# Kernel tuning notes

Hardware: AMD Instinct MI355X
Metric: run time of the kernel (lower is better)

The kernel has to match this reference:

```python
import jax, jax.numpy as jnp
import numpy as np

B, T, I, H, O = 64, 2048, 256, 256, 128

def _rnn_scan(xp, W_hh):
    # xp: [T, B, H] = precomputed W_ih @ x + b_ih + b_hh per timestep
    h0 = jnp.zeros((xp.shape[1], W_hh.shape[0]), xp.dtype)
    def step(h, xt):
        h_new = jnp.tanh(xt + h @ W_hh.T)
        return h_new, h_new
    _, hs = jax.lax.scan(step, h0, xp)
    return hs  # [T, B, H]

def setup_inputs() -> dict:
    key = jax.random.key(0)
    ks = jax.random.split(key, 9)
    s1 = 1.0 / np.sqrt(H)
    s2 = 1.0 / np.sqrt(O)
    return {
        "x": jax.random.normal(ks[0], (B, T, I), dtype=jnp.float32),
        "W_ih1": jax.random.normal(ks[1], (H, I), dtype=jnp.float32) * s1,
        "W_hh1": jax.random.normal(ks[2], (H, H), dtype=jnp.float32) * s1,
        "b_ih1": jax.random.normal(ks[3], (H,), dtype=jnp.float32) * s1,
        "b_hh1": jax.random.normal(ks[4], (H,), dtype=jnp.float32) * s1,
        "W_ih2": jax.random.normal(ks[5], (O, H), dtype=jnp.float32) * s2,
        "W_hh2": jax.random.normal(ks[6], (O, O), dtype=jnp.float32) * s2,
        "b_ih2": jax.random.normal(ks[7], (O,), dtype=jnp.float32) * s2,
        "b_hh2": jax.random.normal(ks[8], (O,), dtype=jnp.float32) * s2,
    }

def reference(x, W_ih1, W_hh1, b_ih1, b_hh1, W_ih2, W_hh2, b_ih2, b_hh2):
    # Layer 1: h_t = tanh(W_ih1 x_t + b_ih1 + W_hh1 h_{t-1} + b_hh1)
    xp1 = jnp.einsum('bti,hi->tbh', x, W_ih1) + (b_ih1 + b_hh1)
    h1 = _rnn_scan(xp1, W_hh1)                      # [T, B, H]
    # Layer 2: o_t = tanh(W_ih2 h_t + b_ih2 + W_hh2 o_{t-1} + b_hh2)
    xp2 = jnp.einsum('tbh,oh->tbo', h1, W_ih2) + (b_ih2 + b_hh2)
    h2 = _rnn_scan(xp2, W_hh2)                      # [T, B, O]
    out = jnp.transpose(h2, (1, 0, 2)).reshape(-1, O)  # [B*T, num_classes]
    return out
```

## Files before the change

kernel.cpp:

```cpp
#include <hip/hip_runtime.h>
#include <math.h>

#define BB 64
#define TT 2048
#define II 256
#define HH 256
#define OO 128

template<int N>
__global__ __launch_bounds__(256)
void gemm_bias(const float* __restrict__ A, const float* __restrict__ W,
               const float* __restrict__ b1, const float* __restrict__ b2,
               float* __restrict__ C)
{
    constexpr int K = 256;
    __shared__ float sA[16][132];
    __shared__ float sB[16][132];
    const int tid  = threadIdx.x;
    const long row0 = (long)blockIdx.x * 128;
    const int  col0 = blockIdx.y * 128;

    const int tm = tid & 15;
    const int tn = tid >> 4;

    float acc[8][8];
#pragma unroll
    for (int i = 0; i < 8; ++i)
#pragma unroll
        for (int j = 0; j < 8; ++j) acc[i][j] = 0.f;

    const int f0  = tid;
    const int f1  = tid + 256;
    const int am0 = f0 >> 2, ak0 = (f0 & 3) * 4;
    const int am1 = f1 >> 2, ak1 = (f1 & 3) * 4;

    for (int kt = 0; kt < K; kt += 16) {
        float4 a0 = *(const float4*)&A[(row0 + am0) * K + kt + ak0];
        float4 a1 = *(const float4*)&A[(row0 + am1) * K + kt + ak1];
        float4 w0 = *(const float4*)&W[(long)(col0 + am0) * K + kt + ak0];
        float4 w1 = *(const float4*)&W[(long)(col0 + am1) * K + kt + ak1];
        __syncthreads();
        sA[ak0+0][am0] = a0.x; sA[ak0+1][am0] = a0.y; sA[ak0+2][am0] = a0.z; sA[ak0+3][am0] = a0.w;
        sA[ak1+0][am1] = a1.x; sA[ak1+1][am1] = a1.y; sA[ak1+2][am1] = a1.z; sA[ak1+3][am1] = a1.w;
        sB[ak0+0][am0] = w0.x; sB[ak0+1][am0] = w0.y; sB[ak0+2][am0] = w0.z; sB[ak0+3][am0] = w0.w;
        sB[ak1+0][am1] = w1.x; sB[ak1+1][am1] = w1.y; sB[ak1+2][am1] = w1.z; sB[ak1+3][am1] = w1.w;
        __syncthreads();
#pragma unroll
        for (int k = 0; k < 16; ++k) {
            float4 av0 = *(const float4*)&sA[k][tm * 8];
            float4 av1 = *(const float4*)&sA[k][tm * 8 + 4];
            float4 bv0 = *(const float4*)&sB[k][tn * 8];
            float4 bv1 = *(const float4*)&sB[k][tn * 8 + 4];
            float am[8] = {av0.x, av0.y, av0.z, av0.w, av1.x, av1.y, av1.z, av1.w};
            float bn[8] = {bv0.x, bv0.y, bv0.z, bv0.w, bv1.x, bv1.y, bv1.z, bv1.w};
#pragma unroll
            for (int i = 0; i < 8; ++i)
#pragma unroll
                for (int j = 0; j < 8; ++j)
                    acc[i][j] += am[i] * bn[j];
        }
    }

    float bias[8];
#pragma unroll
    for (int j = 0; j < 8; ++j) {
        int col = col0 + tn * 8 + j;
        bias[j] = b1[col] + b2[col];
    }
#pragma unroll
    for (int i = 0; i < 8; ++i) {
        long row = row0 + tm * 8 + i;
        float4 v0, v1;
        v0.x = acc[i][0] + bias[0]; v0.y = acc[i][1] + bias[1];
        v0.z = acc[i][2] + bias[2]; v0.w = acc[i][3] + bias[3];
        v1.x = acc[i][4] + bias[4]; v1.y = acc[i][5] + bias[5];
        v1.z = acc[i][6] + bias[6]; v1.w = acc[i][7] + bias[7];
        *(float4*)&C[row * N + col0 + tn * 8]     = v0;
        *(float4*)&C[row * N + col0 + tn * 8 + 4] = v1;
    }
}

__device__ __forceinline__ float fast_tanh(float x) {
    float e = __expf(2.f * x);
    return 1.f - 2.f / (e + 1.f);
}

#define LIGHT_BARRIER() do {                                       \
    asm volatile("s_waitcnt lgkmcnt(0)" ::: "memory");             \
    __builtin_amdgcn_s_barrier();                                  \
} while (0)

#define PIN4(v) asm volatile("" : "+v"((v).x), "+v"((v).y), "+v"((v).z), "+v"((v).w))

#define FMA1(acc_, w_, h_) \
    asm("v_fma_f32 %0, %1, %2, %0" : "+v"(acc_) : "v"(w_), "v"(h_))

#define PAIRSUM(dst_, x_) do {                                         \
    float _t = (x_), _u = (x_);                                        \
    asm("v_permlane32_swap_b32 %0, %1" : "+v"(_t), "+v"(_u));          \
    (dst_) = _t + _u;                                                  \
} while (0)

__global__ __launch_bounds__(512, 2)
void rnn_pipe(const float* __restrict__ W_hh1,
              const float* __restrict__ W_ih2,
              const float* __restrict__ W_hh2,
              const float* __restrict__ b_ih2,
              const float* __restrict__ b_hh2,
              float* __restrict__ XH,
              float* __restrict__ out,
              int* __restrict__ flags)
{
    const int tid = threadIdx.x;
    const int g   = tid & 31;
    const int ks  = tid >> 5;
    const int kp  = ks >> 1;

    if (blockIdx.x < BB) {
        __shared__ float h_lds[256];
        __shared__ float part[8 * 256];
        const int b = blockIdx.x;

        float4 w[8][4];
#pragma unroll
        for (int r = 0; r < 8; ++r)
#pragma unroll
            for (int c = 0; c < 4; ++c)
                w[r][c] = *(const float4*)&W_hh1[(g * 8 + r) * 256 + ks * 16 + c * 4];
#pragma unroll
        for (int r = 0; r < 8; ++r)
#pragma unroll
            for (int c = 0; c < 4; ++c)
                PIN4(w[r][c]);

        float* rowp = XH + (long)b * TT * HH;
        float xpb[4] = {0.f, 0.f, 0.f, 0.f};
        if (tid < 256) {
            h_lds[tid] = 0.f;
#pragma unroll
            for (int j = 0; j < 4; ++j) xpb[j] = rowp[(long)j * HH + tid];
        }
        const int ro = ((tid & 7) >> 2) * 128 + ((tid >> 3) << 2) + (tid & 3);
        LIGHT_BARRIER();

        for (int t0 = 0; t0 < TT; t0 += 4) {
#pragma unroll
            for (int j = 0; j < 4; ++j) {
                const int t = t0 + j;

                float a[8];
#pragma unroll
                for (int r = 0; r < 8; ++r) a[r] = 0.f;
#pragma unroll
                for (int c = 0; c < 4; ++c) {
                    float4 h4c = *(const float4*)&h_lds[ks * 16 + c * 4];
#pragma unroll
                    for (int r = 0; r < 8; ++r) {
                        FMA1(a[r], w[r][c].x, h4c.x);
                        FMA1(a[r], w[r][c].y, h4c.y);
                        FMA1(a[r], w[r][c].z, h4c.z);
                        FMA1(a[r], w[r][c].w, h4c.w);
                    }
                }

                float s[8];
#pragma unroll
                for (int r = 0; r < 8; ++r) PAIRSUM(s[r], a[r]);

                if (!(ks & 1))
                    *(float4*)&part[kp * 256 + g * 4] =
                        make_float4(s[0], s[1], s[2], s[3]);
                else
                    *(float4*)&part[kp * 256 + 128 + g * 4] =
                        make_float4(s[4], s[5], s[6], s[7]);
                LIGHT_BARRIER();

                if (tid < 256) {
                    float s0 = part[0 * 256 + ro] + part[1 * 256 + ro]
                             + part[2 * 256 + ro] + part[3 * 256 + ro];
                    float s1 = part[4 * 256 + ro] + part[5 * 256 + ro]
                             + part[6 * 256 + ro] + part[7 * 256 + ro];
                    float v = fast_tanh((s0 + s1) + xpb[j]);
                    h_lds[tid] = v;
                    rowp[(long)t * HH + tid] = v;
                }
                if (j < 3) LIGHT_BARRIER();
            }

            if (((t0 + 4) & 7) == 0) {
                asm volatile("s_waitcnt vmcnt(0) lgkmcnt(0)" ::: "memory");
                __builtin_amdgcn_s_barrier();
                if (tid == 0)
                    __hip_atomic_store(&flags[b], t0 + 4, __ATOMIC_RELEASE,
                                       __HIP_MEMORY_SCOPE_AGENT);
            } else {
                LIGHT_BARRIER();
            }

            if (tid < 256 && t0 + 4 < TT) {
#pragma unroll
                for (int j = 0; j < 4; ++j)
                    xpb[j] = rowp[(long)(t0 + 4 + j) * HH + tid];
            }
        }
    } else {
        __shared__ float h1_lds[256];
        __shared__ float o_lds[128];
        __shared__ float part2[8 * 132];
        __shared__ int   seen_sh;
        const int b = blockIdx.x - BB;

        float4 wi[4][4];
        float4 wh[4][2];
#pragma unroll
        for (int r = 0; r < 4; ++r) {
#pragma unroll
            for (int c = 0; c < 4; ++c)
                wi[r][c] = *(const float4*)&W_ih2[(g * 4 + r) * 256 + ks * 16 + c * 4];
#pragma unroll
            for (int c = 0; c < 2; ++c)
                wh[r][c] = *(const float4*)&W_hh2[(g * 4 + r) * 128 + ks * 8 + c * 4];
        }
#pragma unroll
        for (int r = 0; r < 4; ++r) {
#pragma unroll
            for (int c = 0; c < 4; ++c) PIN4(wi[r][c]);
#pragma unroll
            for (int c = 0; c < 2; ++c) PIN4(wh[r][c]);
        }

        float bias = 0.f;
        if (tid < 128) {
            bias = b_ih2[tid] + b_hh2[tid];
            o_lds[tid] = 0.f;
        }
        const float* h1p = XH + (long)b * TT * HH;
        float* outp      = out + (long)b * TT * OO;
        LIGHT_BARRIER();

        int seen = 0;
        for (int t = 0; t < TT; ++t) {
            if (seen <= t) {
                if (tid == 0) {
                    int s;
                    do {
                        s = __hip_atomic_load(&flags[b], __ATOMIC_RELAXED,
                                              __HIP_MEMORY_SCOPE_AGENT);
                    } while (s <= t);
                    s = __hip_atomic_load(&flags[b], __ATOMIC_ACQUIRE,
                                          __HIP_MEMORY_SCOPE_AGENT);
                    seen_sh = s;
                }
                LIGHT_BARRIER();
                seen = seen_sh;
            }
            if (tid < 64)
                *(float4*)&h1_lds[tid * 4] = *(const float4*)&h1p[(long)t * HH + tid * 4];
            LIGHT_BARRIER();

            float a2[4];
#pragma unroll
            for (int r = 0; r < 4; ++r) a2[r] = 0.f;
#pragma unroll
            for (int c = 0; c < 4; ++c) {
                float4 h4c = *(const float4*)&h1_lds[ks * 16 + c * 4];
#pragma unroll
                for (int r = 0; r < 4; ++r) {
                    FMA1(a2[r], wi[r][c].x, h4c.x);
                    FMA1(a2[r], wi[r][c].y, h4c.y);
                    FMA1(a2[r], wi[r][c].z, h4c.z);
                    FMA1(a2[r], wi[r][c].w, h4c.w);
                }
            }
#pragma unroll
            for (int c = 0; c < 2; ++c) {
                float4 o4c = *(const float4*)&o_lds[ks * 8 + c * 4];
#pragma unroll
                for (int r = 0; r < 4; ++r) {
                    FMA1(a2[r], wh[r][c].x, o4c.x);
                    FMA1(a2[r], wh[r][c].y, o4c.y);
                    FMA1(a2[r], wh[r][c].z, o4c.z);
                    FMA1(a2[r], wh[r][c].w, o4c.w);
                }
            }

            float s2[4];
#pragma unroll
            for (int r = 0; r < 4; ++r) PAIRSUM(s2[r], a2[r]);

            if (!(ks & 1))
                *(float4*)&part2[kp * 132 + g * 4] =
                    make_float4(s2[0], s2[1], s2[2], s2[3]);
            LIGHT_BARRIER();

            if (tid < 128) {
                float s = bias;
#pragma unroll
                for (int st = 0; st < 8; ++st)
                    s += part2[st * 132 + tid];
                float v = fast_tanh(s);
                o_lds[tid] = v;
                outp[(long)t * OO + tid] = v;
            }
        }
    }
}

extern "C" void kernel_launch(void* const* d_in, const int* in_sizes, int n_in,
                              void* d_out, int out_size, void* d_ws, size_t ws_size,
                              hipStream_t stream)
{
    const float* x     = (const float*)d_in[0];
    const float* W_ih1 = (const float*)d_in[1];
    const float* W_hh1 = (const float*)d_in[2];
    const float* b_ih1 = (const float*)d_in[3];
    const float* b_hh1 = (const float*)d_in[4];
    const float* W_ih2 = (const float*)d_in[5];
    const float* W_hh2 = (const float*)d_in[6];
    const float* b_ih2 = (const float*)d_in[7];
    const float* b_hh2 = (const float*)d_in[8];
    float* out = (float*)d_out;

    float* xp1 = (float*)d_ws;
    const size_t FLAG_OFF = (size_t)BB * TT * HH * sizeof(float);
    int* flags = (int*)((char*)d_ws + FLAG_OFF);

    const int M = BB * TT;

    (void)hipMemsetAsync(flags, 0, BB * sizeof(int), stream);

    dim3 gA(M / 128, HH / 128);
    gemm_bias<HH><<<gA, 256, 0, stream>>>(x, W_ih1, b_ih1, b_hh1, xp1);

    rnn_pipe<<<2 * BB, 512, 0, stream>>>(W_hh1, W_ih2, W_hh2, b_ih2, b_hh2,
                                         xp1, out, flags);
}
```

Baseline: 2.028 ms.

## Batch layer-1 steps by eight, prefetch h1 in layer 2, use nontemporal memory ops

Layer 1 now unrolls eight timesteps per outer iteration instead of four. It prefetches eight xp values and publishes its progress flag once per eight steps, which removes the alternating light/full barrier logic. Layer 2 waits on the flag once per eight-step chunk and software-prefetches the next h1 row from global memory while the current step computes. Both layers switch hand-written v_fma asm to plain C expressions and use nontemporal loads and stores. The compiler may reassociate the dot-product sums differently, and the extra registers for xpb[8] and prefetch could add pressure.

```diff
diff --git a/kernel.cpp b/kernel.cpp
--- a/kernel.cpp
+++ b/kernel.cpp
@@ -6,6 +6,8 @@
 #define II 256
 #define HH 256
 #define OO 128
+
+typedef __attribute__((ext_vector_type(4))) float f32x4;
 
 template<int N>
 __global__ __launch_bounds__(256)
@@ -91,9 +93,6 @@
 } while (0)
 
 #define PIN4(v) asm volatile("" : "+v"((v).x), "+v"((v).y), "+v"((v).z), "+v"((v).w))
-
-#define FMA1(acc_, w_, h_) \
-    asm("v_fma_f32 %0, %1, %2, %0" : "+v"(acc_) : "v"(w_), "v"(h_))
 
 #define PAIRSUM(dst_, x_) do {                                         \
     float _t = (x_), _u = (x_);                                        \
@@ -134,18 +133,21 @@
                 PIN4(w[r][c]);
 
         float* rowp = XH + (long)b * TT * HH;
-        float xpb[4] = {0.f, 0.f, 0.f, 0.f};
+        float xpb[8];
+#pragma unroll
+        for (int j = 0; j < 8; ++j) xpb[j] = 0.f;
         if (tid < 256) {
             h_lds[tid] = 0.f;
 #pragma unroll
-            for (int j = 0; j < 4; ++j) xpb[j] = rowp[(long)j * HH + tid];
+            for (int j = 0; j < 8; ++j)
+                xpb[j] = __builtin_nontemporal_load(&rowp[(long)j * HH + tid]);
         }
         const int ro = ((tid & 7) >> 2) * 128 + ((tid >> 3) << 2) + (tid & 3);
         LIGHT_BARRIER();
 
-        for (int t0 = 0; t0 < TT; t0 += 4) {
-#pragma unroll
-            for (int j = 0; j < 4; ++j) {
+        for (int t0 = 0; t0 < TT; t0 += 8) {
+#pragma unroll
+            for (int j = 0; j < 8; ++j) {
                 const int t = t0 + j;
 
                 float a[8];
@@ -155,12 +157,9 @@
                 for (int c = 0; c < 4; ++c) {
                     float4 h4c = *(const float4*)&h_lds[ks * 16 + c * 4];
 #pragma unroll
-                    for (int r = 0; r < 8; ++r) {
-                        FMA1(a[r], w[r][c].x, h4c.x);
-                        FMA1(a[r], w[r][c].y, h4c.y);
-                        FMA1(a[r], w[r][c].z, h4c.z);
-                        FMA1(a[r], w[r][c].w, h4c.w);
-                    }
+                    for (int r = 0; r < 8; ++r)
+                        a[r] += w[r][c].x * h4c.x + w[r][c].y * h4c.y
+                              + w[r][c].z * h4c.z + w[r][c].w * h4c.w;
                 }
 
                 float s[8];
@@ -176,31 +175,28 @@
                 LIGHT_BARRIER();
 
                 if (tid < 256) {
-                    float s0 = part[0 * 256 + ro] + part[1 * 256 + ro]
+                    float r0 = part[0 * 256 + ro] + part[1 * 256 + ro]
                              + part[2 * 256 + ro] + part[3 * 256 + ro];
-                    float s1 = part[4 * 256 + ro] + part[5 * 256 + ro]
+                    float r1 = part[4 * 256 + ro] + part[5 * 256 + ro]
                              + part[6 * 256 + ro] + part[7 * 256 + ro];
-                    float v = fast_tanh((s0 + s1) + xpb[j]);
+                    float v = fast_tanh((r0 + r1) + xpb[j]);
                     h_lds[tid] = v;
-                    rowp[(long)t * HH + tid] = v;
-                }
-                if (j < 3) LIGHT_BARRIER();
+                    __builtin_nontemporal_store(v, &rowp[(long)t * HH + tid]);
+                }
+                if (j < 7) LIGHT_BARRIER();
             }
 
-            if (((t0 + 4) & 7) == 0) {
-                asm volatile("s_waitcnt vmcnt(0) lgkmcnt(0)" ::: "memory");
-                __builtin_amdgcn_s_barrier();
-                if (tid == 0)
-                    __hip_atomic_store(&flags[b], t0 + 4, __ATOMIC_RELEASE,
-                                       __HIP_MEMORY_SCOPE_AGENT);
-            } else {
-                LIGHT_BARRIER();
-            }
-
-            if (tid < 256 && t0 + 4 < TT) {
-#pragma unroll
-                for (int j = 0; j < 4; ++j)
-                    xpb[j] = rowp[(long)(t0 + 4 + j) * HH + tid];
+            asm volatile("s_waitcnt vmcnt(0) lgkmcnt(0)" ::: "memory");
+            __builtin_amdgcn_s_barrier();
+            if (tid == 0)
+                __hip_atomic_store(&flags[b], t0 + 8, __ATOMIC_RELEASE,
+                                   __HIP_MEMORY_SCOPE_AGENT);
+
+            if (tid < 256 && t0 + 8 < TT) {
+#pragma unroll
+                for (int j = 0; j < 8; ++j)
+                    xpb[j] = __builtin_nontemporal_load(
+                        &rowp[(long)(t0 + 8 + j) * HH + tid]);
             }
         }
     } else {
@@ -239,14 +235,15 @@
         LIGHT_BARRIER();
 
         int seen = 0;
-        for (int t = 0; t < TT; ++t) {
-            if (seen <= t) {
+        f32x4 pf = {0.f, 0.f, 0.f, 0.f};
+        for (int t0 = 0; t0 < TT; t0 += 8) {
+            if (seen < t0 + 8) {
                 if (tid == 0) {
                     int s;
                     do {
                         s = __hip_atomic_load(&flags[b], __ATOMIC_RELAXED,
                                               __HIP_MEMORY_SCOPE_AGENT);
-                    } while (s <= t);
+                    } while (s < t0 + 8);
                     s = __hip_atomic_load(&flags[b], __ATOMIC_ACQUIRE,
                                           __HIP_MEMORY_SCOPE_AGENT);
                     seen_sh = s;
@@ -255,52 +252,57 @@
                 seen = seen_sh;
             }
             if (tid < 64)
-                *(float4*)&h1_lds[tid * 4] = *(const float4*)&h1p[(long)t * HH + tid * 4];
-            LIGHT_BARRIER();
-
-            float a2[4];
-#pragma unroll
-            for (int r = 0; r < 4; ++r) a2[r] = 0.f;
-#pragma unroll
-            for (int c = 0; c < 4; ++c) {
-                float4 h4c = *(const float4*)&h1_lds[ks * 16 + c * 4];
-#pragma unroll
-                for (int r = 0; r < 4; ++r) {
-                    FMA1(a2[r], wi[r][c].x, h4c.x);
-                    FMA1(a2[r], wi[r][c].y, h4c.y);
-                    FMA1(a2[r], wi[r][c].z, h4c.z);
-                    FMA1(a2[r], wi[r][c].w, h4c.w);
-                }
-            }
-#pragma unroll
-            for (int c = 0; c < 2; ++c) {
-                float4 o4c = *(const float4*)&o_lds[ks * 8 + c * 4];
-#pragma unroll
-                for (int r = 0; r < 4; ++r) {
-                    FMA1(a2[r], wh[r][c].x, o4c.x);
-                    FMA1(a2[r], wh[r][c].y, o4c.y);
-                    FMA1(a2[r], wh[r][c].z, o4c.z);
-                    FMA1(a2[r], wh[r][c].w, o4c.w);
-                }
-            }
-
-            float s2[4];
-#pragma unroll
-            for (int r = 0; r < 4; ++r) PAIRSUM(s2[r], a2[r]);
-
-            if (!(ks & 1))
-                *(float4*)&part2[kp * 132 + g * 4] =
-                    make_float4(s2[0], s2[1], s2[2], s2[3]);
-            LIGHT_BARRIER();
-
-            if (tid < 128) {
-                float s = bias;
-#pragma unroll
-                for (int st = 0; st < 8; ++st)
-                    s += part2[st * 132 + tid];
-                float v = fast_tanh(s);
-                o_lds[tid] = v;
-                outp[(long)t * OO + tid] = v;
+                pf = __builtin_nontemporal_load(
+                    (const f32x4*)&h1p[(long)t0 * HH + tid * 4]);
+
+            for (int j = 0; j < 8; ++j) {
+                const int t = t0 + j;
+                if (tid < 64) {
+                    *(f32x4*)&h1_lds[tid * 4] = pf;
+                    if (j < 7)
+                        pf = __builtin_nontemporal_load(
+                            (const f32x4*)&h1p[(long)(t + 1) * HH + tid * 4]);
+                }
+                LIGHT_BARRIER();
+
+                float a2[4];
+#pragma unroll
+                for (int r = 0; r < 4; ++r) a2[r] = 0.f;
+#pragma unroll
+                for (int c = 0; c < 4; ++c) {
+                    float4 h4c = *(const float4*)&h1_lds[ks * 16 + c * 4];
+#pragma unroll
+                    for (int r = 0; r < 4; ++r)
+                        a2[r] += wi[r][c].x * h4c.x + wi[r][c].y * h4c.y
+                               + wi[r][c].z * h4c.z + wi[r][c].w * h4c.w;
+                }
+#pragma unroll
+                for (int c = 0; c < 2; ++c) {
+                    float4 o4c = *(const float4*)&o_lds[ks * 8 + c * 4];
+#pragma unroll
+                    for (int r = 0; r < 4; ++r)
+                        a2[r] += wh[r][c].x * o4c.x + wh[r][c].y * o4c.y
+                               + wh[r][c].z * o4c.z + wh[r][c].w * o4c.w;
+                }
+
+                float s2[4];
+#pragma unroll
+                for (int r = 0; r < 4; ++r) PAIRSUM(s2[r], a2[r]);
+
+                if (!(ks & 1))
+                    *(float4*)&part2[kp * 132 + g * 4] =
+                        make_float4(s2[0], s2[1], s2[2], s2[3]);
+                LIGHT_BARRIER();
+
+                if (tid < 128) {
+                    float s = bias;
+#pragma unroll
+                    for (int st = 0; st < 8; ++st)
+                        s += part2[st * 132 + tid];
+                    float v = fast_tanh(s);
+                    o_lds[tid] = v;
+                    __builtin_nontemporal_store(v, &outp[(long)t * OO + tid]);
+                }
             }
         }
     }
```

After: 2.043 ms. About the same (+0.8%).
